# Optimization experiments

Hardware: AMD Instinct MI355X
Metric: run time of the kernel (lower is better)

The kernel has to match this reference:

```python
import jax, jax.numpy as jnp
import numpy as np


def setup_inputs() -> dict:
    key = jax.random.key(0)
    x = jax.random.normal(key, (8192, 24576), dtype=jnp.float32)
    return {"x": x, "k": 64}


def reference(x, k):
    # torch.topk(x, k, dim=-1) -> indices of k largest per row
    _, k_inds = jax.lax.top_k(x, k)  # [batch, k]
    batch = x.shape[0]
    rows = jnp.arange(batch)[:, None]  # [batch, 1], broadcasts against [batch, k]
    # mask = zeros_like(x).scatter_(-1, k_inds, ones)
    mask = jnp.zeros_like(x).at[rows, k_inds].set(1.0)
    return mask * x
```

## Files before the change

### kernel.cpp

```cpp
#include <hip/hip_runtime.h>


#define COLS  24576
#define TPB   1024
#define NCH   6
#define EPT   24
#define NSUB  32
#define HPAD  257

typedef float v4f __attribute__((ext_vector_type(4)));

__device__ __forceinline__ unsigned int f2o(unsigned int b) {
    return (b & 0x80000000u) ? ~b : (b | 0x80000000u);
}
__device__ __forceinline__ float o2f(unsigned int u) {
    unsigned int b = (u & 0x80000000u) ? (u & 0x7fffffffu) : ~u;
    return __uint_as_float(b);
}

extern "C" __global__ __launch_bounds__(TPB, 8)
void topk_mask(const float* __restrict__ x, const int* __restrict__ kptr,
               float* __restrict__ out)
{
    __shared__ unsigned int whist[NSUB * HPAD];
    __shared__ unsigned int hist[256];
    __shared__ unsigned int sb, sr, scnt;

    const int t    = threadIdx.x;
    const int lane = t & 63;
    const int wave = t >> 6;
    const long long row = blockIdx.x;

    const unsigned int k = (unsigned int)kptr[0];

    for (int i = t; i < NSUB * HPAD; i += TPB) whist[i] = 0u;

    const v4f* rp = (const v4f*)(x + row * COLS);
    unsigned int uu[EPT];
    #pragma unroll
    for (int j = 0; j < NCH; j++) {
        v4f v = __builtin_nontemporal_load(rp + j * TPB + t);
        uu[4*j+0] = f2o(__float_as_uint(v.x));
        uu[4*j+1] = f2o(__float_as_uint(v.y));
        uu[4*j+2] = f2o(__float_as_uint(v.z));
        uu[4*j+3] = f2o(__float_as_uint(v.w));
    }
    __syncthreads();

    unsigned int* myh = &whist[(((unsigned)wave << 1) | (unsigned)(lane & 1)) * HPAD];
    #pragma unroll
    for (int e = 0; e < EPT; e++) atomicAdd(&myh[uu[e] >> 24], 1u);
    __syncthreads();

    if (t < 256) {
        unsigned int s = 0;
        #pragma unroll
        for (int h = 0; h < NSUB; h++) s += whist[h * HPAD + t];
        hist[t] = s;
    }
    __syncthreads();

    auto scan_select = [&](unsigned int rr) {
        unsigned int c0 = hist[4*lane+0], c1 = hist[4*lane+1];
        unsigned int c2 = hist[4*lane+2], c3 = hist[4*lane+3];
        unsigned int gs = c0 + c1 + c2 + c3;
        unsigned int s = gs;
        #pragma unroll
        for (int d = 1; d < 64; d <<= 1) {
            unsigned int o = __shfl_down(s, d);
            s += (lane + d < 64) ? o : 0u;
        }
        unsigned int T = s - gs;
        if (T < rr && rr <= T + gs) {
            unsigned int A = T, b, c;
            if (A + c3 >= rr)                { b = 3; c = c3; }
            else if (A + c3 + c2 >= rr)      { A += c3;           b = 2; c = c2; }
            else if (A + c3 + c2 + c1 >= rr) { A += c3 + c2;      b = 1; c = c1; }
            else                             { A += c3 + c2 + c1; b = 0; c = c0; }
            sb   = 4u * (unsigned)lane + b;
            sr   = rr - A;
            scnt = c;
        }
    };

    unsigned int r = k;
    if (wave == 0) scan_select(r);
    __syncthreads();
    unsigned int pref = sb;
    r = sr;

    #pragma unroll
    for (int shift = 16; shift >= 0; shift -= 8) {
        if (t < 256) hist[t] = 0u;
        __syncthreads();
        #pragma unroll
        for (int e = 0; e < EPT; e++) {
            unsigned int u = uu[e];
            if ((u >> (shift + 8)) == pref)
                atomicAdd(&hist[(u >> shift) & 255u], 1u);
        }
        __syncthreads();
        if (wave == 0) scan_select(r);
        __syncthreads();
        pref = (pref << 8) | sb;
        r = sr;
    }

    const unsigned int u_t  = pref;
    const unsigned int need = r;
    const unsigned int eq   = scnt;

    unsigned int m = COLS;
    if (eq != need) {
        unsigned int lo = 0, hi = COLS;
        while (hi - lo > 1u) {
            unsigned int mid = (lo + hi) >> 1;
            __syncthreads();
            if (t == 0) hist[0] = 0u;
            __syncthreads();
            unsigned int loc = 0;
            #pragma unroll
            for (int j = 0; j < NCH; j++) {
                #pragma unroll
                for (int q = 0; q < 4; q++) {
                    unsigned int col = (unsigned)(j * (TPB * 4) + (t << 2) + q);
                    loc += (uu[4*j+q] == u_t && col < mid) ? 1u : 0u;
                }
            }
            if (loc) atomicAdd(&hist[0], loc);
            __syncthreads();
            if (hist[0] >= need) hi = mid; else lo = mid;
        }
        m = hi;
    }

    v4f* op = (v4f*)(out + row * COLS);
    #pragma unroll
    for (int j = 0; j < NCH; j++) {
        unsigned int cbase = (unsigned)(j * (TPB * 4) + (t << 2));
        unsigned int u0 = uu[4*j+0], u1 = uu[4*j+1];
        unsigned int u2 = uu[4*j+2], u3 = uu[4*j+3];
        v4f w;
        w.x = (u0 > u_t || (u0 == u_t && cbase + 0u < m)) ? o2f(u0) : 0.0f;
        w.y = (u1 > u_t || (u1 == u_t && cbase + 1u < m)) ? o2f(u1) : 0.0f;
        w.z = (u2 > u_t || (u2 == u_t && cbase + 2u < m)) ? o2f(u2) : 0.0f;
        w.w = (u3 > u_t || (u3 == u_t && cbase + 3u < m)) ? o2f(u3) : 0.0f;
        __builtin_nontemporal_store(w, op + j * TPB + t);
    }
}

extern "C" void kernel_launch(void* const* d_in, const int* in_sizes, int n_in,
                              void* d_out, int out_size, void* d_ws, size_t ws_size,
                              hipStream_t stream)
{
    const float* x    = (const float*)d_in[0];
    const int*   kptr = (const int*)d_in[1];
    float*       outp = (float*)d_out;
    const int rows = in_sizes[0] / COLS;
    topk_mask<<<rows, TPB, 0, stream>>>(x, kptr, outp);
}
```

Before: 1.309 ms.

## Make topk-mask kernel persistent with async LDS prefetch of the next row

```diff
diff --git a/kernel.cpp b/kernel.cpp
--- a/kernel.cpp
+++ b/kernel.cpp
@@ -7,6 +7,7 @@
 #define EPT   24
 #define NSUB  32
 #define HPAD  257
+#define NBLK  256
 
 typedef float v4f __attribute__((ext_vector_type(4)));
 
@@ -18,10 +19,28 @@
     return __uint_as_float(b);
 }
 
-extern "C" __global__ __launch_bounds__(TPB, 8)
+#define BAR() do { asm volatile("s_waitcnt lgkmcnt(0)" ::: "memory"); \
+                   __builtin_amdgcn_s_barrier();                      \
+                   asm volatile("" ::: "memory"); } while (0)
+
+#define PREFETCH_ROW(rowptr)                                                       \
+    do {                                                                           \
+        const unsigned int* _gp = (const unsigned int*)(rowptr);                   \
+        _Pragma("unroll")                                                          \
+        for (int _j = 0; _j < NCH; _j++) {                                         \
+            const int _i4 = (_j * TPB + t) * 4;                                    \
+            __builtin_amdgcn_global_load_lds(                                      \
+                (const __attribute__((address_space(1))) unsigned int*)(_gp + _i4),\
+                (__attribute__((address_space(3))) unsigned int*)(&stage[_i4]),    \
+                16, 0, 0);                                                         \
+        }                                                                          \
+    } while (0)
+
+extern "C" __global__ __launch_bounds__(TPB, 4)
 void topk_mask(const float* __restrict__ x, const int* __restrict__ kptr,
-               float* __restrict__ out)
+               float* __restrict__ out, int nrows, int rpb)
 {
+    __shared__ __align__(16) unsigned int stage[COLS];
     __shared__ unsigned int whist[NSUB * HPAD];
     __shared__ unsigned int hist[256];
     __shared__ unsigned int sb, sr, scnt;
@@ -29,36 +48,10 @@
     const int t    = threadIdx.x;
     const int lane = t & 63;
     const int wave = t >> 6;
-    const long long row = blockIdx.x;
+    const unsigned int k = (unsigned int)kptr[0];
+    const long long row0 = (long long)blockIdx.x * rpb;
 
-    const unsigned int k = (unsigned int)kptr[0];
-
-    for (int i = t; i < NSUB * HPAD; i += TPB) whist[i] = 0u;
-
-    const v4f* rp = (const v4f*)(x + row * COLS);
-    unsigned int uu[EPT];
-    #pragma unroll
-    for (int j = 0; j < NCH; j++) {
-        v4f v = __builtin_nontemporal_load(rp + j * TPB + t);
-        uu[4*j+0] = f2o(__float_as_uint(v.x));
-        uu[4*j+1] = f2o(__float_as_uint(v.y));
-        uu[4*j+2] = f2o(__float_as_uint(v.z));
-        uu[4*j+3] = f2o(__float_as_uint(v.w));
-    }
-    __syncthreads();
-
-    unsigned int* myh = &whist[(((unsigned)wave << 1) | (unsigned)(lane & 1)) * HPAD];
-    #pragma unroll
-    for (int e = 0; e < EPT; e++) atomicAdd(&myh[uu[e] >> 24], 1u);
-    __syncthreads();
-
-    if (t < 256) {
-        unsigned int s = 0;
-        #pragma unroll
-        for (int h = 0; h < NSUB; h++) s += whist[h * HPAD + t];
-        hist[t] = s;
-    }
-    __syncthreads();
+    if (row0 < nrows) PREFETCH_ROW(x + row0 * COLS);
 
     auto scan_select = [&](unsigned int rr) {
         unsigned int c0 = hist[4*lane+0], c1 = hist[4*lane+1];
@@ -83,69 +76,111 @@
         }
     };
 
-    unsigned int r = k;
-    if (wave == 0) scan_select(r);
-    __syncthreads();
-    unsigned int pref = sb;
-    r = sr;
+    for (int i = 0; i < rpb; i++) {
+        const long long row = row0 + i;
+        if (row >= nrows) break;
 
-    #pragma unroll
-    for (int shift = 16; shift >= 0; shift -= 8) {
-        if (t < 256) hist[t] = 0u;
-        __syncthreads();
+        asm volatile("s_waitcnt vmcnt(0)" ::: "memory");
+        __builtin_amdgcn_sched_barrier(0);
+
+        unsigned int uu[EPT];
         #pragma unroll
-        for (int e = 0; e < EPT; e++) {
-            unsigned int u = uu[e];
-            if ((u >> (shift + 8)) == pref)
-                atomicAdd(&hist[(u >> shift) & 255u], 1u);
+        for (int j = 0; j < NCH; j++) {
+            const uint4 v = *(const uint4*)&stage[(j * TPB + t) * 4];
+            uu[4*j+0] = f2o(v.x); uu[4*j+1] = f2o(v.y);
+            uu[4*j+2] = f2o(v.z); uu[4*j+3] = f2o(v.w);
         }
-        __syncthreads();
+        asm volatile("s_waitcnt lgkmcnt(0)" ::: "memory");
+        __builtin_amdgcn_sched_barrier(0);
+
+        if (i + 1 < rpb && row + 1 < nrows) PREFETCH_ROW(x + (row + 1) * COLS);
+
+        {
+            unsigned int* wz = &whist[(wave * 2) * HPAD];
+            #pragma unroll
+            for (int q = 0; q < (2 * HPAD + 63) / 64; q++) {
+                int idx = q * 64 + lane;
+                if (idx < 2 * HPAD) wz[idx] = 0u;
+            }
+        }
+
+        unsigned int* myh = &whist[(((unsigned)wave << 1) | (unsigned)(lane & 1)) * HPAD];
+        #pragma unroll
+        for (int e = 0; e < EPT; e++) atomicAdd(&myh[uu[e] >> 24], 1u);
+        BAR();
+
+        if (t < 256) {
+            unsigned int s = 0;
+            #pragma unroll
+            for (int h = 0; h < NSUB; h++) s += whist[h * HPAD + t];
+            hist[t] = s;
+        }
+        BAR();
+
+        unsigned int r = k;
         if (wave == 0) scan_select(r);
-        __syncthreads();
-        pref = (pref << 8) | sb;
+        BAR();
+        unsigned int pref = sb;
         r = sr;
-    }
 
-    const unsigned int u_t  = pref;
-    const unsigned int need = r;
-    const unsigned int eq   = scnt;
+        #pragma unroll
+        for (int shift = 16; shift >= 0; shift -= 8) {
+            if (t < 256) hist[t] = 0u;
+            BAR();
+            #pragma unroll
+            for (int e = 0; e < EPT; e++) {
+                unsigned int u = uu[e];
+                if ((u >> (shift + 8)) == pref)
+                    atomicAdd(&hist[(u >> shift) & 255u], 1u);
+            }
+            BAR();
+            if (wave == 0) scan_select(r);
+            BAR();
+            pref = (pref << 8) | sb;
+            r = sr;
+        }
 
-    unsigned int m = COLS;
-    if (eq != need) {
-        unsigned int lo = 0, hi = COLS;
-        while (hi - lo > 1u) {
-            unsigned int mid = (lo + hi) >> 1;
-            __syncthreads();
-            if (t == 0) hist[0] = 0u;
-            __syncthreads();
-            unsigned int loc = 0;
-            #pragma unroll
-            for (int j = 0; j < NCH; j++) {
+        const unsigned int u_t  = pref;
+        const unsigned int need = r;
+        const unsigned int eq   = scnt;
+
+        unsigned int m = COLS;
+        if (eq != need) {
+            unsigned int lo = 0, hi = COLS;
+            while (hi - lo > 1u) {
+                unsigned int mid = (lo + hi) >> 1;
+                BAR();
+                if (t == 0) hist[0] = 0u;
+                BAR();
+                unsigned int loc = 0;
                 #pragma unroll
-                for (int q = 0; q < 4; q++) {
-                    unsigned int col = (unsigned)(j * (TPB * 4) + (t << 2) + q);
-                    loc += (uu[4*j+q] == u_t && col < mid) ? 1u : 0u;
+                for (int j = 0; j < NCH; j++) {
+                    #pragma unroll
+                    for (int q = 0; q < 4; q++) {
+                        unsigned int col = (unsigned)(j * (TPB * 4) + (t << 2) + q);
+                        loc += (uu[4*j+q] == u_t && col < mid) ? 1u : 0u;
+                    }
                 }
+                if (loc) atomicAdd(&hist[0], loc);
+                BAR();
+                if (hist[0] >= need) hi = mid; else lo = mid;
             }
-            if (loc) atomicAdd(&hist[0], loc);
-            __syncthreads();
-            if (hist[0] >= need) hi = mid; else lo = mid;
+            m = hi;
         }
-        m = hi;
-    }
 
-    v4f* op = (v4f*)(out + row * COLS);
-    #pragma unroll
-    for (int j = 0; j < NCH; j++) {
-        unsigned int cbase = (unsigned)(j * (TPB * 4) + (t << 2));
-        unsigned int u0 = uu[4*j+0], u1 = uu[4*j+1];
-        unsigned int u2 = uu[4*j+2], u3 = uu[4*j+3];
-        v4f w;
-        w.x = (u0 > u_t || (u0 == u_t && cbase + 0u < m)) ? o2f(u0) : 0.0f;
-        w.y = (u1 > u_t || (u1 == u_t && cbase + 1u < m)) ? o2f(u1) : 0.0f;
-        w.z = (u2 > u_t || (u2 == u_t && cbase + 2u < m)) ? o2f(u2) : 0.0f;
-        w.w = (u3 > u_t || (u3 == u_t && cbase + 3u < m)) ? o2f(u3) : 0.0f;
-        __builtin_nontemporal_store(w, op + j * TPB + t);
+        v4f* op = (v4f*)(out + row * COLS);
+        #pragma unroll
+        for (int j = 0; j < NCH; j++) {
+            unsigned int cbase = (unsigned)(j * (TPB * 4) + (t << 2));
+            unsigned int u0 = uu[4*j+0], u1 = uu[4*j+1];
+            unsigned int u2 = uu[4*j+2], u3 = uu[4*j+3];
+            v4f w;
+            w.x = (u0 > u_t || (u0 == u_t && cbase + 0u < m)) ? o2f(u0) : 0.0f;
+            w.y = (u1 > u_t || (u1 == u_t && cbase + 1u < m)) ? o2f(u1) : 0.0f;
+            w.z = (u2 > u_t || (u2 == u_t && cbase + 2u < m)) ? o2f(u2) : 0.0f;
+            w.w = (u3 > u_t || (u3 == u_t && cbase + 3u < m)) ? o2f(u3) : 0.0f;
+            __builtin_nontemporal_store(w, op + j * TPB + t);
+        }
     }
 }
 
@@ -157,5 +192,6 @@
     const int*   kptr = (const int*)d_in[1];
     float*       outp = (float*)d_out;
     const int rows = in_sizes[0] / COLS;
-    topk_mask<<<rows, TPB, 0, stream>>>(x, kptr, outp);
+    const int rpb  = (rows + NBLK - 1) / NBLK;
+    topk_mask<<<NBLK, TPB, 0, stream>>>(x, kptr, outp, rows, rpb);
 }
```

Result: slower. 1.386 ms (+5.9%).
